# Kernel tuning notes

Hardware: AMD Instinct MI355X
Metric: run time of the kernel (lower is better)

The kernel has to match this reference:

```python
import jax, jax.numpy as jnp
import numpy as np

N = 100000      # nodes
E = 1600000     # edges (before self-loops)
F_IN = 128      # num_node_features
H = 8           # heads in conv1
C = 16          # per-head channels in conv1 (hard-coded in module)
K = 32          # num_classes (conv2 out, single head)
NEG_SLOPE = 0.2 # PyG GATConv default


def setup_inputs() -> dict:
    key = jax.random.key(0)
    ks = jax.random.split(key, 8)
    x = jax.random.normal(ks[0], (N, F_IN), dtype=jnp.float32)
    edge_index = jax.random.randint(ks[1], (2, E), 0, N, dtype=jnp.int32)
    # conv1 params (Glorot-ish scale)
    W1 = jax.random.normal(ks[2], (H * C, F_IN), dtype=jnp.float32) / np.sqrt(F_IN)
    att_src1 = jax.random.normal(ks[3], (H, C), dtype=jnp.float32) / np.sqrt(C)
    att_dst1 = jax.random.normal(ks[4], (H, C), dtype=jnp.float32) / np.sqrt(C)
    b1 = jnp.zeros((H * C,), dtype=jnp.float32)
    # conv2 params (heads=1)
    W2 = jax.random.normal(ks[5], (K, H * C), dtype=jnp.float32) / np.sqrt(H * C)
    att_src2 = jax.random.normal(ks[6], (1, K), dtype=jnp.float32) / np.sqrt(K)
    att_dst2 = jax.random.normal(ks[7], (1, K), dtype=jnp.float32) / np.sqrt(K)
    b2 = jnp.zeros((K,), dtype=jnp.float32)
    return {"inputs": x, "edge_index": edge_index,
            "W1": W1, "att_src1": att_src1, "att_dst1": att_dst1, "b1": b1,
            "W2": W2, "att_src2": att_src2, "att_dst2": att_dst2, "b2": b2}


def gat_conv(x, src, dst, W, a_src, a_dst, bias, heads, ch):
    # x: [N, F_in]; src/dst: [E2] (self-loops already appended)
    h = (x @ W.T).reshape(N, heads, ch)                  # [N, H, C]
    al_s = (h * a_src[None]).sum(-1)                     # [N, H]
    al_d = (h * a_dst[None]).sum(-1)                     # [N, H]
    e = al_s[src] + al_d[dst]                            # [E2, H]
    e = jnp.where(e >= 0, e, NEG_SLOPE * e)              # LeakyReLU
    # segment softmax over edges sharing a destination node
    m = jax.ops.segment_max(e, dst, num_segments=N)      # [N, H]
    p = jnp.exp(e - m[dst])
    s = jax.ops.segment_sum(p, dst, num_segments=N)
    alpha = p / (s[dst] + 1e-16)                         # [E2, H]
    msg = h[src] * alpha[:, :, None]                     # [E2, H, C]
    out = jax.ops.segment_sum(msg, dst, num_segments=N)  # [N, H, C]
    return out.reshape(N, heads * ch) + bias, alpha


def reference(inputs, edge_index, W1, att_src1, att_dst1, b1, W2, att_src2, att_dst2, b2):
    loop = jnp.arange(N, dtype=edge_index.dtype)
    src = jnp.concatenate([edge_index[0], loop])         # add self-loops
    dst = jnp.concatenate([edge_index[1], loop])
    x1, _ = gat_conv(inputs, src, dst, W1, att_src1, att_dst1, b1, H, C)
    x1 = jax.nn.relu(x1)                                 # [N, H*C]
    x2, alpha = gat_conv(x1, src, dst, W2, att_src2, att_dst2, b2, 1, K)
    edge_index_new = jnp.stack([src, dst])               # [2, E+N]
    return x2, edge_index_new, alpha
```

## Files before the change

### kernel.cpp

```cpp
#include <hip/hip_runtime.h>
#include <hip/hip_bf16.h>
#include <cstdint>
#include <cstddef>

#define NN  100000
#define EE  1600000
#define NE2 1700000
#define NBINS 391
#define BCAP  8192
#define EPB   16384
#define NBINBLK ((NE2 + EPB - 1) / EPB)

#define OUT_X2    3200000
#define OUT_ALPHA 6600000

__device__ __forceinline__ float lrelu(float v) { return v >= 0.f ? v : 0.2f * v; }

typedef float v2f __attribute__((ext_vector_type(2)));
typedef short short8 __attribute__((ext_vector_type(8)));
typedef float f32x4 __attribute__((ext_vector_type(4)));

__device__ __forceinline__ unsigned cvtpk_bf16(float lo, float hi) {
  unsigned r;
  asm("v_cvt_pk_bf16_f32 %0, %1, %2" : "=v"(r) : "v"(lo), "v"(hi));
  return r;
}

#if __has_builtin(__builtin_amdgcn_cvt_pk_f32_fp8) && __has_builtin(__builtin_amdgcn_cvt_pk_fp8_f32)
#define HW_FP8 1
#endif

__device__ __forceinline__ float fp8dec1(unsigned b) {
  unsigned e = (b >> 3) & 15, m = b & 7;
  float v = e ? __uint_as_float(((e + 120u) << 23) | (m << 20))
              : (float)m * 0.001953125f;
  return (b & 0x80u) ? -v : v;
}
__device__ __forceinline__ unsigned fp8enc1(float x) {
  unsigned s = x < 0.f ? 0x80u : 0u;
  float a = fminf(fabsf(x), 448.f);
  if (a < 0.0009765625f) return s;
  unsigned ub = __float_as_uint(a);
  int ex = (int)(ub >> 23) - 127;
  if (ex < -6) {
    unsigned m = (unsigned)(a * 512.f + 0.5f);
    return s | (m > 7u ? 7u : m);
  }
  float sc = __uint_as_float((unsigned)(127 - ex) << 23);
  unsigned m = (unsigned)((a * sc - 1.f) * 8.f + 0.5f);
  if (m == 8u) { m = 0u; ++ex; }
  if (ex > 8) { ex = 8; m = 7u; }
  return s | ((unsigned)(ex + 7) << 3) | m;
}

template <bool HI>
__device__ __forceinline__ v2f fp8x2(unsigned u) {
#ifdef HW_FP8
  return __builtin_amdgcn_cvt_pk_f32_fp8((int)u, HI);
#else
  unsigned w = HI ? (u >> 16) : u;
  v2f r; r.x = fp8dec1(w & 255u); r.y = fp8dec1((w >> 8) & 255u);
  return r;
#endif
}
__device__ __forceinline__ unsigned packfp8x4(float a, float b, float c, float d) {
#ifdef HW_FP8
  int r = __builtin_amdgcn_cvt_pk_fp8_f32(a, b, 0, false);
  r = __builtin_amdgcn_cvt_pk_fp8_f32(c, d, r, true);
  return (unsigned)r;
#else
  return fp8enc1(a) | (fp8enc1(b) << 8) | (fp8enc1(c) << 16) | (fp8enc1(d) << 24);
#endif
}

__device__ __forceinline__ void acc16(float w, uint4 u,
    float4& A, float4& B, float4& C, float4& D)
{
  v2f p;
  p = fp8x2<false>(u.x); A.x += w * p.x; A.y += w * p.y;
  p = fp8x2<true >(u.x); A.z += w * p.x; A.w += w * p.y;
  p = fp8x2<false>(u.y); B.x += w * p.x; B.y += w * p.y;
  p = fp8x2<true >(u.y); B.z += w * p.x; B.w += w * p.y;
  p = fp8x2<false>(u.z); C.x += w * p.x; C.y += w * p.y;
  p = fp8x2<true >(u.z); C.z += w * p.x; C.w += w * p.y;
  p = fp8x2<false>(u.w); D.x += w * p.x; D.y += w * p.y;
  p = fp8x2<true >(u.w); D.z += w * p.x; D.w += w * p.y;
}

__global__ __launch_bounds__(256) void k_gemm1(
    const float* __restrict__ x, const float* __restrict__ W1,
    const float* __restrict__ a_src, const float* __restrict__ a_dst,
    unsigned* __restrict__ h1f8, float* __restrict__ als, float* __restrict__ ald)
{
  __shared__ __align__(16) char lds[49152];
  char* xs_c = lds;
  char* Wb_c = lds + 16384;
  float* Cl  = (float*)lds;

  const int t = threadIdx.x;
  const int row0 = blockIdx.x * 64;

  #pragma unroll
  for (int i = 0; i < 16; ++i) {
    int idx4 = i * 256 + t;
    int n = idx4 >> 5, kq = idx4 & 31;
    float4 v = ((const float4*)W1)[idx4];
    unsigned lo = cvtpk_bf16(v.x, v.y), hi = cvtpk_bf16(v.z, v.w);
    int byte = n * 256 + ((((kq >> 1) ^ (n & 7)) << 4) | ((kq & 1) << 3));
    *(uint2*)(Wb_c + byte) = make_uint2(lo, hi);
  }
  #pragma unroll
  for (int i = 0; i < 8; ++i) {
    int idx4 = i * 256 + t;
    int r = idx4 >> 5, kq = idx4 & 31;
    int grow = row0 + r;
    float4 v = (grow < NN) ? ((const float4*)x)[(size_t)grow * 32 + kq]
                           : make_float4(0.f, 0.f, 0.f, 0.f);
    unsigned lo = cvtpk_bf16(v.x, v.y), hi = cvtpk_bf16(v.z, v.w);
    int byte = r * 256 + ((((kq >> 1) ^ (r & 7)) << 4) | ((kq & 1) << 3));
    *(uint2*)(xs_c + byte) = make_uint2(lo, hi);
  }
  __syncthreads();

  const int w = t >> 6, l = t & 63, m = l & 15, g = l >> 4;
  f32x4 acc[8] = {};
  const char* xrow = xs_c + (16 * w + m) * 256;
  #pragma unroll
  for (int kk = 0; kk < 4; ++kk) {
    int chunk = (((kk << 2) + g) ^ (m & 7)) << 4;
    short8 av = *(const short8*)(xrow + chunk);
    #pragma unroll
    for (int nb = 0; nb < 8; ++nb) {
      short8 bv = *(const short8*)(Wb_c + (16 * nb + m) * 256 + chunk);
      acc[nb] = __builtin_amdgcn_mfma_f32_16x16x32_bf16(av, bv, acc[nb], 0, 0, 0);
    }
  }

  __syncthreads();
  #pragma unroll
  for (int nb = 0; nb < 8; ++nb)
    #pragma unroll
    for (int j = 0; j < 4; ++j)
      Cl[(16 * w + 4 * g + j) * 128 + 16 * nb + m] = acc[nb][j];
  __syncthreads();

  const int cg = t & 31, rg = t >> 5;
  float4 sA = ((const float4*)a_src)[cg];
  float4 dA = ((const float4*)a_dst)[cg];
  #pragma unroll
  for (int j = 0; j < 8; ++j) {
    int r = 8 * rg + j;
    int grow = row0 + r;
    if (grow >= NN) break;
    float4 cv = *(const float4*)&Cl[r * 128 + 4 * cg];
    h1f8[(size_t)grow * 32 + cg] = packfp8x4(cv.x, cv.y, cv.z, cv.w);
    float ps = cv.x * sA.x + cv.y * sA.y + cv.z * sA.z + cv.w * sA.w;
    float pd = cv.x * dA.x + cv.y * dA.y + cv.z * dA.z + cv.w * dA.w;
    ps += __shfl_xor(ps, 1); ps += __shfl_xor(ps, 2);
    pd += __shfl_xor(pd, 1); pd += __shfl_xor(pd, 2);
    if ((cg & 3) == 0) {
      als[(size_t)grow * 8 + (cg >> 2)] = ps;
      ald[(size_t)grow * 8 + (cg >> 2)] = pd;
    }
  }
}

__global__ __launch_bounds__(1024) void k_bin(
    const int* __restrict__ ei, int* __restrict__ bincnt,
    unsigned* __restrict__ binbuf, float* __restrict__ out)
{
  __shared__ int hist[NBINS];
  __shared__ int bbase[NBINS];
  const int t = threadIdx.x;
  const int e0 = blockIdx.x * EPB;
  const int rep = blockIdx.x & 1;
  int* bc = bincnt + rep * NBINS;
  unsigned* bb = binbuf + (size_t)rep * NBINS * BCAP;

  int mybin[16];
  unsigned mypay[16];

  for (int i = t; i < NBINS; i += 1024) hist[i] = 0;
  __syncthreads();

  #pragma unroll
  for (int k = 0; k < 16; ++k) {
    int i = e0 + k * 1024 + t;
    int b = -1; unsigned pay = 0;
    if (i < NE2) {
      int src, dst;
      if (i < EE) { src = ei[i]; dst = ei[EE + i]; } else { src = dst = i - EE; }
      out[OUT_X2 + i] = (float)src;
      out[OUT_X2 + NE2 + i] = (float)dst;
      b = dst >> 8;
      pay = ((unsigned)src << 8) | (dst & 255);
      atomicAdd(&hist[b], 1);
    }
    mybin[k] = b; mypay[k] = pay;
  }
  __syncthreads();

  for (int i = t; i < NBINS; i += 1024) {
    int c = hist[i];
    bbase[i] = c ? atomicAdd(&bc[i], c) : 0;
    hist[i] = 0;
  }
  __syncthreads();

  #pragma unroll
  for (int k = 0; k < 16; ++k) {
    int b = mybin[k];
    if (b >= 0) {
      int pos = bbase[b] + atomicAdd(&hist[b], 1);
      if (pos < BCAP) bb[(size_t)b * BCAP + pos] = mypay[k];
    }
  }
}

__global__ __launch_bounds__(512) void k_binscan(
    const int* __restrict__ bincnt, int* __restrict__ binstart)
{
  __shared__ int tmp[512];
  int t = threadIdx.x;
  int v = (t < NBINS) ? (bincnt[t] + bincnt[NBINS + t]) : 0;
  tmp[t] = v;
  __syncthreads();
  #pragma unroll
  for (int off = 1; off < 512; off <<= 1) {
    int add = (t >= off) ? tmp[t - off] : 0;
    __syncthreads();
    tmp[t] += add;
    __syncthreads();
  }
  if (t < NBINS) binstart[t] = tmp[t] - v;
}

__global__ __launch_bounds__(256) void k_binsort(
    const unsigned* __restrict__ binbuf, const int* __restrict__ bincnt,
    const int* __restrict__ binstart, int* __restrict__ base,
    int* __restrict__ csr)
{
  __shared__ int deg[256];
  __shared__ int sc[256];
  __shared__ int cur[256];
  const int b = blockIdx.x;
  const int t = threadIdx.x;
  const int cntA = bincnt[b];
  const int cntB = bincnt[NBINS + b];
  const int start = binstart[b];
  const unsigned* bufA = binbuf + (size_t)b * BCAP;
  const unsigned* bufB = binbuf + (size_t)(NBINS + b) * BCAP;

  deg[t] = 0;
  __syncthreads();
  for (int i = t; i < cntA; i += 256) atomicAdd(&deg[bufA[i] & 255], 1);
  for (int i = t; i < cntB; i += 256) atomicAdd(&deg[bufB[i] & 255], 1);
  __syncthreads();

  sc[t] = deg[t];
  __syncthreads();
  #pragma unroll
  for (int off = 1; off < 256; off <<= 1) {
    int add = (t >= off) ? sc[t - off] : 0;
    __syncthreads();
    sc[t] += add;
    __syncthreads();
  }
  int excl = sc[t] - deg[t];

  int node = b * 256 + t;
  if (node < NN) base[node] = start + excl;
  if (b == NBINS - 1 && t == 0) base[NN] = NE2;
  cur[t] = excl;
  __syncthreads();

  for (int i = t; i < cntA; i += 256) {
    unsigned u = bufA[i];
    int pos = atomicAdd(&cur[u & 255], 1);
    csr[start + pos] = (int)(u >> 8);
  }
  for (int i = t; i < cntB; i += 256) {
    unsigned u = bufB[i];
    int pos = atomicAdd(&cur[u & 255], 1);
    csr[start + pos] = (int)(u >> 8);
  }
}

__global__ __launch_bounds__(256) void k_node1(
    const int* __restrict__ base, const int* __restrict__ csr_src,
    const float* __restrict__ als, const float* __restrict__ ald,
    const uint4* __restrict__ h1x4, uint4* __restrict__ acc1x4)
{
  int gid = blockIdx.x * 256 + threadIdx.x;
  int node = gid >> 3;
  int q = gid & 7;
  float ad = ald[(size_t)node * 8 + q];
  int s0 = base[node], s1 = base[node + 1];
  float4 A = {0,0,0,0}, B = {0,0,0,0}, C = {0,0,0,0}, D = {0,0,0,0};
  float sw = 0.f;
  int i = s0;
  int n4 = s0 + ((s1 - s0) & ~3);
  int c0 = 0, c1 = 0, c2 = 0, c3 = 0;
  if (i < n4) {
    c0 = csr_src[i]; c1 = csr_src[i + 1];
    c2 = csr_src[i + 2]; c3 = csr_src[i + 3];
  }
  while (i < n4) {
    int src0 = c0, src1 = c1, src2 = c2, src3 = c3;
    int ni = i + 4;
    if (ni < n4) {
      c0 = csr_src[ni]; c1 = csr_src[ni + 1];
      c2 = csr_src[ni + 2]; c3 = csr_src[ni + 3];
    }
    float e0 = als[(size_t)src0 * 8 + q] + ad;
    float e1 = als[(size_t)src1 * 8 + q] + ad;
    float e2 = als[(size_t)src2 * 8 + q] + ad;
    float e3 = als[(size_t)src3 * 8 + q] + ad;
    uint4 u0 = h1x4[(size_t)src0 * 8 + q];
    uint4 u1 = h1x4[(size_t)src1 * 8 + q];
    uint4 u2 = h1x4[(size_t)src2 * 8 + q];
    uint4 u3 = h1x4[(size_t)src3 * 8 + q];
    float w0 = __expf(lrelu(e0));
    float w1 = __expf(lrelu(e1));
    float w2 = __expf(lrelu(e2));
    float w3 = __expf(lrelu(e3));
    acc16(w0, u0, A, B, C, D);
    acc16(w1, u1, A, B, C, D);
    acc16(w2, u2, A, B, C, D);
    acc16(w3, u3, A, B, C, D);
    sw += w0 + w1 + w2 + w3;
    i = ni;
  }
  for (; i < s1; ++i) {
    int src = csr_src[i];
    float w = __expf(lrelu(als[(size_t)src * 8 + q] + ad));
    uint4 u = h1x4[(size_t)src * 8 + q];
    acc16(w, u, A, B, C, D);
    sw += w;
  }
  float inv = 1.f / (sw + 1e-16f);
  uint4 o;
  o.x = packfp8x4(A.x * inv, A.y * inv, A.z * inv, A.w * inv);
  o.y = packfp8x4(B.x * inv, B.y * inv, B.z * inv, B.w * inv);
  o.z = packfp8x4(C.x * inv, C.y * inv, C.z * inv, C.w * inv);
  o.w = packfp8x4(D.x * inv, D.y * inv, D.z * inv, D.w * inv);
  acc1x4[(size_t)node * 8 + q] = o;
}

__global__ __launch_bounds__(256) void k_gemm2(
    const unsigned* __restrict__ acc1f8, const float* __restrict__ b1,
    const float* __restrict__ W2, const float* __restrict__ a_src,
    const float* __restrict__ a_dst,
    unsigned* __restrict__ h2f8, float* __restrict__ als, float* __restrict__ ald)
{
  __shared__ float Wt[128 * 32];
  __shared__ float xs[64 * 132];
  const int t = threadIdx.x;
  const int row0 = blockIdx.x * 64;

  {
    const float4* W4 = (const float4*)W2;
    #pragma unroll
    for (int i = 0; i < 4; ++i) {
      int idx4 = t * 4 + i;
      int c = idx4 >> 5, f4 = idx4 & 31;
      float4 v = W4[idx4];
      Wt[(4 * f4 + 0) * 32 + c] = v.x;
      Wt[(4 * f4 + 1) * 32 + c] = v.y;
      Wt[(4 * f4 + 2) * 32 + c] = v.z;
      Wt[(4 * f4 + 3) * 32 + c] = v.w;
    }
  }
  #pragma unroll
  for (int i = 0; i < 8; ++i) {
    int idx = i * 256 + t;
    int r = idx >> 5, u = idx & 31;
    int grow = row0 + r;
    unsigned v = (grow < NN) ? acc1f8[(size_t)grow * 32 + u] : 0u;
    float4 bb = ((const float4*)b1)[u];
    v2f lo = fp8x2<false>(v), hi = fp8x2<true>(v);
    xs[r * 132 + 4 * u + 0] = fmaxf(lo.x + bb.x, 0.f);
    xs[r * 132 + 4 * u + 1] = fmaxf(lo.y + bb.y, 0.f);
    xs[r * 132 + 4 * u + 2] = fmaxf(hi.x + bb.z, 0.f);
    xs[r * 132 + 4 * u + 3] = fmaxf(hi.y + bb.w, 0.f);
  }
  __syncthreads();

  const int c4 = t & 7;
  const int rg = t >> 3;
  float acc[2][4];
  #pragma unroll
  for (int j = 0; j < 2; ++j)
    #pragma unroll
    for (int k = 0; k < 4; ++k) acc[j][k] = 0.f;

  const float4* Wt4 = (const float4*)Wt;
  #pragma unroll 4
  for (int f = 0; f < 128; ++f) {
    float4 wv = Wt4[f * 8 + c4];
    #pragma unroll
    for (int j = 0; j < 2; ++j) {
      float xv = xs[(2 * rg + j) * 132 + f];
      acc[j][0] += xv * wv.x; acc[j][1] += xv * wv.y;
      acc[j][2] += xv * wv.z; acc[j][3] += xv * wv.w;
    }
  }

  float4 sv = ((const float4*)a_src)[c4];
  float4 dv = ((const float4*)a_dst)[c4];
  #pragma unroll
  for (int j = 0; j < 2; ++j) {
    int grow = row0 + 2 * rg + j;
    if (grow < NN) {
      h2f8[(size_t)grow * 8 + c4] = packfp8x4(acc[j][0], acc[j][1], acc[j][2], acc[j][3]);
      float ps = acc[j][0] * sv.x + acc[j][1] * sv.y + acc[j][2] * sv.z + acc[j][3] * sv.w;
      float pd = acc[j][0] * dv.x + acc[j][1] * dv.y + acc[j][2] * dv.z + acc[j][3] * dv.w;
      ps += __shfl_xor(ps, 1); ps += __shfl_xor(ps, 2); ps += __shfl_xor(ps, 4);
      pd += __shfl_xor(pd, 1); pd += __shfl_xor(pd, 2); pd += __shfl_xor(pd, 4);
      if (c4 == 0) { als[grow] = ps; ald[grow] = pd; }
    }
  }
}

__global__ __launch_bounds__(256) void k_node2(
    const int* __restrict__ base, const int* __restrict__ csr_src,
    const float* __restrict__ als, const float* __restrict__ ald,
    const uint2* __restrict__ h2x2, const float* __restrict__ b2,
    float* __restrict__ out_x2, float* __restrict__ s2)
{
  int gid = blockIdx.x * 256 + threadIdx.x;
  int node = gid >> 2, j = gid & 3;
  if (node >= NN) return;
  float ad = ald[node];
  int s0 = base[node], s1 = base[node + 1];
  float4 A = {0,0,0,0}, B = {0,0,0,0};
  float sw = 0.f;
  int i = s0;
  int n4 = s0 + ((s1 - s0) & ~3);
  for (; i < n4; i += 4) {
    int src0 = csr_src[i + 0];
    int src1 = csr_src[i + 1];
    int src2 = csr_src[i + 2];
    int src3 = csr_src[i + 3];
    float e0 = als[src0] + ad;
    float e1 = als[src1] + ad;
    float e2 = als[src2] + ad;
    float e3 = als[src3] + ad;
    uint2 u0 = h2x2[(size_t)src0 * 4 + j];
    uint2 u1 = h2x2[(size_t)src1 * 4 + j];
    uint2 u2 = h2x2[(size_t)src2 * 4 + j];
    uint2 u3 = h2x2[(size_t)src3 * 4 + j];
    float w0 = __expf(lrelu(e0));
    float w1 = __expf(lrelu(e1));
    float w2 = __expf(lrelu(e2));
    float w3 = __expf(lrelu(e3));
    { v2f p;
      p = fp8x2<false>(u0.x); A.x += w0 * p.x; A.y += w0 * p.y;
      p = fp8x2<true >(u0.x); A.z += w0 * p.x; A.w += w0 * p.y;
      p = fp8x2<false>(u0.y); B.x += w0 * p.x; B.y += w0 * p.y;
      p = fp8x2<true >(u0.y); B.z += w0 * p.x; B.w += w0 * p.y; }
    { v2f p;
      p = fp8x2<false>(u1.x); A.x += w1 * p.x; A.y += w1 * p.y;
      p = fp8x2<true >(u1.x); A.z += w1 * p.x; A.w += w1 * p.y;
      p = fp8x2<false>(u1.y); B.x += w1 * p.x; B.y += w1 * p.y;
      p = fp8x2<true >(u1.y); B.z += w1 * p.x; B.w += w1 * p.y; }
    { v2f p;
      p = fp8x2<false>(u2.x); A.x += w2 * p.x; A.y += w2 * p.y;
      p = fp8x2<true >(u2.x); A.z += w2 * p.x; A.w += w2 * p.y;
      p = fp8x2<false>(u2.y); B.x += w2 * p.x; B.y += w2 * p.y;
      p = fp8x2<true >(u2.y); B.z += w2 * p.x; B.w += w2 * p.y; }
    { v2f p;
      p = fp8x2<false>(u3.x); A.x += w3 * p.x; A.y += w3 * p.y;
      p = fp8x2<true >(u3.x); A.z += w3 * p.x; A.w += w3 * p.y;
      p = fp8x2<false>(u3.y); B.x += w3 * p.x; B.y += w3 * p.y;
      p = fp8x2<true >(u3.y); B.z += w3 * p.x; B.w += w3 * p.y; }
    sw += w0 + w1 + w2 + w3;
  }
  for (; i < s1; ++i) {
    int src = csr_src[i];
    float w = __expf(lrelu(als[src] + ad));
    uint2 u = h2x2[(size_t)src * 4 + j];
    v2f p;
    p = fp8x2<false>(u.x); A.x += w * p.x; A.y += w * p.y;
    p = fp8x2<true >(u.x); A.z += w * p.x; A.w += w * p.y;
    p = fp8x2<false>(u.y); B.x += w * p.x; B.y += w * p.y;
    p = fp8x2<true >(u.y); B.z += w * p.x; B.w += w * p.y;
    sw += w;
  }
  float inv = 1.f / (sw + 1e-16f);
  float4 b0 = ((const float4*)b2)[2 * j];
  float4 b1v = ((const float4*)b2)[2 * j + 1];
  float4* o = (float4*)&out_x2[(size_t)node * 32 + 8 * j];
  o[0] = make_float4(A.x * inv + b0.x, A.y * inv + b0.y,
                     A.z * inv + b0.z, A.w * inv + b0.w);
  o[1] = make_float4(B.x * inv + b1v.x, B.y * inv + b1v.y,
                     B.z * inv + b1v.z, B.w * inv + b1v.w);
  if (j == 0) s2[node] = sw;
}

__global__ __launch_bounds__(256) void k_alpha_edges(
    const int* __restrict__ ei, const float* __restrict__ als,
    const float* __restrict__ ald, const float* __restrict__ s2,
    float* __restrict__ out)
{
  int e = blockIdx.x * 256 + threadIdx.x;
  if (e >= NE2) return;
  int src, dst;
  if (e < EE) { src = ei[e]; dst = ei[EE + e]; } else { src = dst = e - EE; }
  float w = __expf(lrelu(als[src] + ald[dst]));
  out[OUT_ALPHA + e] = w / (s2[dst] + 1e-16f);
}

extern "C" void kernel_launch(void* const* d_in, const int* in_sizes, int n_in,
                              void* d_out, int out_size, void* d_ws, size_t ws_size,
                              hipStream_t stream)
{
  const float* x   = (const float*)d_in[0];
  const int*   ei  = (const int*)d_in[1];
  const float* W1  = (const float*)d_in[2];
  const float* as1 = (const float*)d_in[3];
  const float* ad1 = (const float*)d_in[4];
  const float* b1  = (const float*)d_in[5];
  const float* W2  = (const float*)d_in[6];
  const float* as2 = (const float*)d_in[7];
  const float* ad2 = (const float*)d_in[8];
  const float* b2  = (const float*)d_in[9];
  float* out = (float*)d_out;

  if (ws_size < 70000000) return;

  char* ws = (char*)d_ws;
  unsigned* h1f8    = (unsigned*)(ws + 0);
  unsigned* acc1f8  = (unsigned*)(ws + 12800000);
  float*    als1    = (float*)(ws + 25600000);
  float*    ald1    = (float*)(ws + 28800000);
  unsigned* h2f8    = (unsigned*)(ws + 32000000);
  float*    als2    = (float*)(ws + 35200000);
  float*    ald2    = (float*)(ws + 35600000);
  float*    s2      = (float*)(ws + 36000000);
  int*      bincnt  = (int*)(ws + 36400000);
  int*      binstart= (int*)(ws + 36404096);
  int*      base    = (int*)(ws + 36408192);
  int*      csr     = (int*)(ws + 36808208);
  unsigned* binbuf  = (unsigned*)(ws + 43608208);

  (void)hipMemsetAsync(bincnt, 0, 4096, stream);

  k_bin    <<<NBINBLK, 1024, 0, stream>>>(ei, bincnt, binbuf, out);
  k_binscan<<<1, 512, 0, stream>>>(bincnt, binstart);
  k_binsort<<<NBINS, 256, 0, stream>>>(binbuf, bincnt, binstart, base, csr);

  k_gemm1<<<(NN + 63) / 64, 256, 0, stream>>>(x, W1, as1, ad1, h1f8, als1, ald1);
  k_node1<<<(NN * 8) / 256, 256, 0, stream>>>(base, csr, als1, ald1,
                                              (const uint4*)h1f8, (uint4*)acc1f8);

  k_gemm2<<<(NN + 63) / 64, 256, 0, stream>>>(acc1f8, b1, W2, as2, ad2, h2f8, als2, ald2);
  k_node2<<<(NN * 4 + 255) / 256, 256, 0, stream>>>(base, csr, als2, ald2,
                                                    (const uint2*)h2f8, b2, out, s2);

  k_alpha_edges<<<(NE2 + 255) / 256, 256, 0, stream>>>(ei, als2, ald2, s2, out);
}
```

Measured before the change: 200.6 us.

## Fuse edge binning into GEMM1 launch and fold bin scan into binsort

Edge binning now runs as extra blocks inside the first GEMM kernel, so the bandwidth-bound binning and the compute-bound GEMM overlap within one launch. The separate bin-prefix-scan kernel is removed: each binsort block computes its own start offset by summing the counts of all earlier bins. Bin replicas go from 2 to 8 with smaller per-block edge chunks, which spreads global atomic contention. The trade-offs are redundant prefix work in every binsort block and a BCAP of 1024 per replica that could overflow if one replica's bin receives more edges than that.

```diff
diff --git a/kernel.cpp b/kernel.cpp
--- a/kernel.cpp
+++ b/kernel.cpp
@@ -7,9 +7,11 @@
 #define EE  1600000
 #define NE2 1700000
 #define NBINS 391
-#define BCAP  8192
-#define EPB   16384
-#define NBINBLK ((NE2 + EPB - 1) / EPB)
+#define NREP  8
+#define BCAP  1024
+#define EPB   4096
+#define NBINBLK 416
+#define NG1BLK  1563
 
 #define OUT_X2    3200000
 #define OUT_ALPHA 6600000
@@ -87,18 +89,69 @@
   p = fp8x2<true >(u.w); D.z += w * p.x; D.w += w * p.y;
 }
 
-__global__ __launch_bounds__(256) void k_gemm1(
+__global__ __launch_bounds__(256) void k_bin_gemm1(
+    const int* __restrict__ ei, int* __restrict__ bincnt,
+    unsigned* __restrict__ binbuf, float* __restrict__ out,
     const float* __restrict__ x, const float* __restrict__ W1,
     const float* __restrict__ a_src, const float* __restrict__ a_dst,
     unsigned* __restrict__ h1f8, float* __restrict__ als, float* __restrict__ ald)
 {
   __shared__ __align__(16) char lds[49152];
+  const int t = threadIdx.x;
+
+  if (blockIdx.x < NBINBLK) {
+    int* hist  = (int*)lds;
+    int* bbase = hist + NBINS;
+    const int e0 = blockIdx.x * EPB;
+    const int rep = blockIdx.x & (NREP - 1);
+    int* bc = bincnt + rep * NBINS;
+    unsigned* bb = binbuf + (size_t)rep * NBINS * BCAP;
+
+    int mybin[16];
+    unsigned mypay[16];
+
+    for (int i = t; i < NBINS; i += 256) hist[i] = 0;
+    __syncthreads();
+
+    #pragma unroll
+    for (int k = 0; k < 16; ++k) {
+      int i = e0 + k * 256 + t;
+      int b = -1; unsigned pay = 0;
+      if (i < NE2) {
+        int src, dst;
+        if (i < EE) { src = ei[i]; dst = ei[EE + i]; } else { src = dst = i - EE; }
+        out[OUT_X2 + i] = (float)src;
+        out[OUT_X2 + NE2 + i] = (float)dst;
+        b = dst >> 8;
+        pay = ((unsigned)src << 8) | (dst & 255);
+        atomicAdd(&hist[b], 1);
+      }
+      mybin[k] = b; mypay[k] = pay;
+    }
+    __syncthreads();
+
+    for (int i = t; i < NBINS; i += 256) {
+      int c = hist[i];
+      bbase[i] = c ? atomicAdd(&bc[i], c) : 0;
+      hist[i] = 0;
+    }
+    __syncthreads();
+
+    #pragma unroll
+    for (int k = 0; k < 16; ++k) {
+      int b = mybin[k];
+      if (b >= 0) {
+        int pos = bbase[b] + atomicAdd(&hist[b], 1);
+        if (pos < BCAP) bb[(size_t)b * BCAP + pos] = mypay[k];
+      }
+    }
+    return;
+  }
+
   char* xs_c = lds;
   char* Wb_c = lds + 16384;
   float* Cl  = (float*)lds;
-
-  const int t = threadIdx.x;
-  const int row0 = blockIdx.x * 64;
+  const int row0 = (blockIdx.x - NBINBLK) * 64;
 
   #pragma unroll
   for (int i = 0; i < 16; ++i) {
@@ -165,96 +218,40 @@
   }
 }
 
-__global__ __launch_bounds__(1024) void k_bin(
-    const int* __restrict__ ei, int* __restrict__ bincnt,
-    unsigned* __restrict__ binbuf, float* __restrict__ out)
-{
-  __shared__ int hist[NBINS];
-  __shared__ int bbase[NBINS];
-  const int t = threadIdx.x;
-  const int e0 = blockIdx.x * EPB;
-  const int rep = blockIdx.x & 1;
-  int* bc = bincnt + rep * NBINS;
-  unsigned* bb = binbuf + (size_t)rep * NBINS * BCAP;
-
-  int mybin[16];
-  unsigned mypay[16];
-
-  for (int i = t; i < NBINS; i += 1024) hist[i] = 0;
-  __syncthreads();
-
-  #pragma unroll
-  for (int k = 0; k < 16; ++k) {
-    int i = e0 + k * 1024 + t;
-    int b = -1; unsigned pay = 0;
-    if (i < NE2) {
-      int src, dst;
-      if (i < EE) { src = ei[i]; dst = ei[EE + i]; } else { src = dst = i - EE; }
-      out[OUT_X2 + i] = (float)src;
-      out[OUT_X2 + NE2 + i] = (float)dst;
-      b = dst >> 8;
-      pay = ((unsigned)src << 8) | (dst & 255);
-      atomicAdd(&hist[b], 1);
-    }
-    mybin[k] = b; mypay[k] = pay;
-  }
-  __syncthreads();
-
-  for (int i = t; i < NBINS; i += 1024) {
-    int c = hist[i];
-    bbase[i] = c ? atomicAdd(&bc[i], c) : 0;
-    hist[i] = 0;
-  }
-  __syncthreads();
-
-  #pragma unroll
-  for (int k = 0; k < 16; ++k) {
-    int b = mybin[k];
-    if (b >= 0) {
-      int pos = bbase[b] + atomicAdd(&hist[b], 1);
-      if (pos < BCAP) bb[(size_t)b * BCAP + pos] = mypay[k];
-    }
-  }
-}
-
-__global__ __launch_bounds__(512) void k_binscan(
-    const int* __restrict__ bincnt, int* __restrict__ binstart)
-{
-  __shared__ int tmp[512];
-  int t = threadIdx.x;
-  int v = (t < NBINS) ? (bincnt[t] + bincnt[NBINS + t]) : 0;
-  tmp[t] = v;
-  __syncthreads();
-  #pragma unroll
-  for (int off = 1; off < 512; off <<= 1) {
-    int add = (t >= off) ? tmp[t - off] : 0;
-    __syncthreads();
-    tmp[t] += add;
-    __syncthreads();
-  }
-  if (t < NBINS) binstart[t] = tmp[t] - v;
-}
-
 __global__ __launch_bounds__(256) void k_binsort(
     const unsigned* __restrict__ binbuf, const int* __restrict__ bincnt,
-    const int* __restrict__ binstart, int* __restrict__ base,
-    int* __restrict__ csr)
+    int* __restrict__ base, int* __restrict__ csr)
 {
   __shared__ int deg[256];
   __shared__ int sc[256];
   __shared__ int cur[256];
   const int b = blockIdx.x;
   const int t = threadIdx.x;
-  const int cntA = bincnt[b];
-  const int cntB = bincnt[NBINS + b];
-  const int start = binstart[b];
-  const unsigned* bufA = binbuf + (size_t)b * BCAP;
-  const unsigned* bufB = binbuf + (size_t)(NBINS + b) * BCAP;
+
+  int acc = 0;
+  #pragma unroll
+  for (int r = 0; r < NREP; ++r)
+    for (int i = t; i < b; i += 256)
+      acc += bincnt[r * NBINS + i];
+  deg[t] = acc;
+  __syncthreads();
+  #pragma unroll
+  for (int off = 128; off >= 1; off >>= 1) {
+    if (t < off) deg[t] += deg[t + off];
+    __syncthreads();
+  }
+  const int start = deg[0];
+  __syncthreads();
 
   deg[t] = 0;
   __syncthreads();
-  for (int i = t; i < cntA; i += 256) atomicAdd(&deg[bufA[i] & 255], 1);
-  for (int i = t; i < cntB; i += 256) atomicAdd(&deg[bufB[i] & 255], 1);
+  #pragma unroll
+  for (int r = 0; r < NREP; ++r) {
+    int cnt = bincnt[r * NBINS + b];
+    const unsigned* buf = binbuf + (size_t)(r * NBINS + b) * BCAP;
+    for (int i = t; i < cnt; i += 256)
+      atomicAdd(&deg[buf[i] & 255], 1);
+  }
   __syncthreads();
 
   sc[t] = deg[t];
@@ -274,15 +271,15 @@
   cur[t] = excl;
   __syncthreads();
 
-  for (int i = t; i < cntA; i += 256) {
-    unsigned u = bufA[i];
-    int pos = atomicAdd(&cur[u & 255], 1);
-    csr[start + pos] = (int)(u >> 8);
-  }
-  for (int i = t; i < cntB; i += 256) {
-    unsigned u = bufB[i];
-    int pos = atomicAdd(&cur[u & 255], 1);
-    csr[start + pos] = (int)(u >> 8);
+  #pragma unroll
+  for (int r = 0; r < NREP; ++r) {
+    int cnt = bincnt[r * NBINS + b];
+    const unsigned* buf = binbuf + (size_t)(r * NBINS + b) * BCAP;
+    for (int i = t; i < cnt; i += 256) {
+      unsigned u = buf[i];
+      int pos = atomicAdd(&cur[u & 255], 1);
+      csr[start + pos] = (int)(u >> 8);
+    }
   }
 }
 
@@ -527,7 +524,7 @@
   const float* b2  = (const float*)d_in[9];
   float* out = (float*)d_out;
 
-  if (ws_size < 70000000) return;
+  if (ws_size < 60000000) return;
 
   char* ws = (char*)d_ws;
   unsigned* h1f8    = (unsigned*)(ws + 0);
@@ -539,18 +536,17 @@
   float*    ald2    = (float*)(ws + 35600000);
   float*    s2      = (float*)(ws + 36000000);
   int*      bincnt  = (int*)(ws + 36400000);
-  int*      binstart= (int*)(ws + 36404096);
-  int*      base    = (int*)(ws + 36408192);
-  int*      csr     = (int*)(ws + 36808208);
-  unsigned* binbuf  = (unsigned*)(ws + 43608208);
-
-  (void)hipMemsetAsync(bincnt, 0, 4096, stream);
-
-  k_bin    <<<NBINBLK, 1024, 0, stream>>>(ei, bincnt, binbuf, out);
-  k_binscan<<<1, 512, 0, stream>>>(bincnt, binstart);
-  k_binsort<<<NBINS, 256, 0, stream>>>(binbuf, bincnt, binstart, base, csr);
-
-  k_gemm1<<<(NN + 63) / 64, 256, 0, stream>>>(x, W1, as1, ad1, h1f8, als1, ald1);
+  int*      base    = (int*)(ws + 36416384);
+  int*      csr     = (int*)(ws + 36816388);
+  unsigned* binbuf  = (unsigned*)(ws + 43616388);
+
+  (void)hipMemsetAsync(bincnt, 0, NREP * NBINS * 4, stream);
+
+  k_bin_gemm1<<<NBINBLK + NG1BLK, 256, 0, stream>>>(
+      ei, bincnt, binbuf, out, x, W1, as1, ad1, h1f8, als1, ald1);
+
+  k_binsort<<<NBINS, 256, 0, stream>>>(binbuf, bincnt, base, csr);
+
   k_node1<<<(NN * 8) / 256, 256, 0, stream>>>(base, csr, als1, ald1,
                                               (const uint4*)h1f8, (uint4*)acc1f8);
 
```

Result: faster. 179.3 us, median of 2 (-10.6%).
